# Optimization experiments

Hardware: AMD Instinct MI355X
Metric: run time of the kernel (lower is better)

The kernel has to match this reference:

```python
import jax, jax.numpy as jnp
import numpy as np

NEAR = 0.01
FAR = 10.0
MAX_ITERS = 32
N_RAYS = 65536
HIDDEN = 128


def setup_inputs() -> dict:
    key = jax.random.key(0)
    ks = jax.random.split(key, 12)
    f = jnp.float32
    origins = jax.random.normal(ks[0], (N_RAYS, 3), f) * 2.0
    directions = jax.random.normal(ks[1], (N_RAYS, 3), f)
    directions = directions / jnp.linalg.norm(directions, axis=-1, keepdims=True)
    s1 = 1.0 / np.sqrt(3.0)
    s2 = 1.0 / np.sqrt(HIDDEN)
    return {
        "origins": origins,
        "directions": directions,
        "W1": jax.random.normal(ks[2], (3, HIDDEN), f) * s1,
        "b1": jax.random.normal(ks[3], (HIDDEN,), f) * 0.01,
        "W2": jax.random.normal(ks[4], (HIDDEN, HIDDEN), f) * s2,
        "b2": jax.random.normal(ks[5], (HIDDEN,), f) * 0.01,
        "W3": jax.random.normal(ks[6], (HIDDEN, 1), f) * s2,
        "b3": jax.random.normal(ks[7], (1,), f) * 0.01,
        "Wc1": jax.random.normal(ks[8], (3, HIDDEN), f) * s1,
        "bc1": jax.random.normal(ks[9], (HIDDEN,), f) * 0.01,
        "Wc2": jax.random.normal(ks[10], (HIDDEN, 3), f) * s2,
        "bc2": jax.random.normal(ks[11], (3,), f) * 0.01,
    }


def reference(origins, directions, W1, b1, W2, b2, W3, b3, Wc1, bc1, Wc2, bc2):
    N = origins.shape[0]

    def sdf(p):  # [N,3] -> [N,1]
        h = jax.nn.relu(p @ W1 + b1)
        h = jax.nn.relu(h @ W2 + b2)
        return h @ W3 + b3

    def get_color(p):  # [N,3] -> [N,3]
        h = jax.nn.relu(p @ Wc1 + bc1)
        return jax.nn.sigmoid(h @ Wc2 + bc2)

    def step(state, _):
        points, distances, final_mask = state
        sdfs = sdf(points)                                  # [N,1]
        valid = (sdfs <= NEAR) & (distances < FAR)          # [N,1] bool
        final_mask = final_mask | valid
        upd = ~valid                                        # rays still marching
        distances = distances + jnp.where(upd, sdfs, 0.0)
        points = points + jnp.where(upd, directions * sdfs, 0.0)
        return (points, distances, final_mask), None

    init = (origins,
            jnp.zeros((N, 1), origins.dtype),
            jnp.zeros((N, 1), dtype=bool))
    (points, distances, final_mask), _ = jax.lax.scan(step, init, None, length=MAX_ITERS)
    final_mask = final_mask | (distances < FAR)             # [N,1]

    # color[mask] = get_color(points[mask]) <=> masked where (get_color is pointwise)
    color = jnp.where(final_mask, get_color(points), 0.0)   # [N,3]
    return color
```

## Files before the change

kernel.cpp:

```cpp
#include <hip/hip_runtime.h>

#define HIDDEN 128
#define N_RAYS 65536
#define NEAR_D 0.01f
#define FAR_D 10.0f
#define MAX_ITERS 32

typedef _Float16 f16x8 __attribute__((ext_vector_type(8)));
typedef float f32x16 __attribute__((ext_vector_type(16)));

template <int CTRL, int ROW_MASK>
__device__ __forceinline__ float dpp_add(float v) {
    int s = __builtin_amdgcn_update_dpp(0, __float_as_int(v), CTRL, ROW_MASK, 0xF, true);
    return v + __int_as_float(s);
}
__device__ __forceinline__ float half_sum_dpp(float v) {
    v = dpp_add<0x111, 0xF>(v);
    v = dpp_add<0x112, 0xF>(v);
    v = dpp_add<0x114, 0xF>(v);
    v = dpp_add<0x118, 0xF>(v);
    v = dpp_add<0x142, 0xA>(v);
    return v;
}

__global__ void w2_frag_kernel(const float* __restrict__ W2,
                               _Float16* __restrict__ img) {
    int tid = blockIdx.x * blockDim.x + threadIdx.x;
    int j = tid & 7;
    int L = (tid >> 3) & 63;
    int tc = tid >> 9;
    int t = tc >> 3, c = tc & 7;
    int n = t * 32 + (L & 31);
    int k = c * 16 + ((L >> 5) & 1) * 8 + j;
    float w = W2[k * HIDDEN + n];
    _Float16 hi = (_Float16)w;
    _Float16 lo = (_Float16)(w - (float)hi);
    img[tid] = hi;
    img[16384 + tid] = lo;
}

__launch_bounds__(256, 2)
__global__ void sphere_trace_kernel(
    const float* __restrict__ origins,
    const float* __restrict__ directions,
    const float* __restrict__ W1,
    const float* __restrict__ b1,
    const _Float16* __restrict__ w2img,
    const float* __restrict__ b2,
    const float* __restrict__ W3,
    const float* __restrict__ b3,
    const float* __restrict__ Wc1,
    const float* __restrict__ bc1,
    const float* __restrict__ Wc2,
    const float* __restrict__ bc2,
    float* __restrict__ out)
{
    __shared__ __align__(16) _Float16 wlds[32768];
    __shared__ float sbuf[4][32];

    const int tid = threadIdx.x;
    const int lane = tid & 63;
    const int w = __builtin_amdgcn_readfirstlane(tid >> 6);
    const int q = lane >> 5;
    const int n32 = lane & 31;

    {
        const float4* src = (const float4*)w2img;
        float4* dst = (float4*)wlds;
        #pragma unroll
        for (int i = 0; i < 16; ++i)
            dst[tid + 256 * i] = src[tid + 256 * i];
    }
    __syncthreads();

    float bAx, bAy, bAz, bB;
    {
        bAx = fmaxf(fabsf(W1[lane]),              fabsf(W1[lane + 64]));
        bAy = fmaxf(fabsf(W1[HIDDEN + lane]),     fabsf(W1[HIDDEN + lane + 64]));
        bAz = fmaxf(fabsf(W1[2 * HIDDEN + lane]), fabsf(W1[2 * HIDDEN + lane + 64]));
        bB  = fmaxf(fabsf(b1[lane]),              fabsf(b1[lane + 64]));
        #pragma unroll
        for (int m = 1; m < 64; m <<= 1) {
            bAx = fmaxf(bAx, __shfl_xor(bAx, m));
            bAy = fmaxf(bAy, __shfl_xor(bAy, m));
            bAz = fmaxf(bAz, __shfl_xor(bAz, m));
            bB  = fmaxf(bB,  __shfl_xor(bB,  m));
        }
    }

    const int ray = blockIdx.x * 128 + w * 32 + n32;
    float px = 0.f, py = 0.f, pz = 0.f, dx = 0.f, dy = 0.f, dz = 0.f;
    float dist = 0.0f;
    bool frozen = true;
    if (lane < 32) {
        px = origins[ray * 3 + 0];
        py = origins[ray * 3 + 1];
        pz = origins[ray * 3 + 2];
        dx = directions[ray * 3 + 0];
        dy = directions[ray * 3 + 1];
        dz = directions[ray * 3 + 2];
        frozen = false;
    }

    float b2v[4], w3v[4];
    #pragma unroll
    for (int t = 0; t < 4; ++t) {
        b2v[t] = b2[t * 32 + n32];
        w3v[t] = W3[t * 32 + n32];
    }
    const float b3v = b3[0];
    const int q8 = q * 8;

    #pragma unroll 1
    for (int it = 0; it < MAX_ITERS; ++it) {
        const float ppx = __shfl(px, n32);
        const float ppy = __shfl(py, n32);
        const float ppz = __shfl(pz, n32);

        const float bound = fmaf(fabsf(ppx), bAx, fmaf(fabsf(ppy), bAy,
                            fmaf(fabsf(ppz), bAz, bB)));
        float sc = 1.0f, inv = 1.0f;
        {
            const int e = (int)((__float_as_uint(bound) >> 23) & 255u);
            if (e > 137) {
                const int sh = e - 137;
                sc  = __uint_as_float((unsigned)(127 - sh) << 23);
                inv = __uint_as_float((unsigned)(127 + sh) << 23);
            }
        }

        f32x16 acc[4];
        #pragma unroll
        for (int t = 0; t < 4; ++t)
            #pragma unroll
            for (int r = 0; r < 16; ++r) acc[t][r] = 0.0f;

        #pragma unroll 1
        for (int c = 0; c < 8; ++c) {
            f16x8 Ah, Al;
            {
                const int kb = c * 16 + q8;
                const float* wpx = W1 + kb;
                const float* wpy = W1 + HIDDEN + kb;
                const float* wpz = W1 + 2 * HIDDEN + kb;
                const float* bp  = b1 + kb;
                #pragma unroll
                for (int jj = 0; jj < 8; ++jj) {
                    const float hv = fmaxf(
                        fmaf(ppx, wpx[jj], fmaf(ppy, wpy[jj],
                        fmaf(ppz, wpz[jj], bp[jj]))), 0.0f);
                    const float x = hv * sc;
                    const _Float16 hi = (_Float16)x;
                    Ah[jj] = hi;
                    Al[jj] = (_Float16)(x - (float)hi);
                }
            }
            #pragma unroll
            for (int t = 0; t < 4; ++t) {
                const int off = ((t * 8 + c) << 9) + (lane << 3);
                const f16x8 bh = *(const f16x8*)(wlds + off);
                const f16x8 bl = *(const f16x8*)(wlds + 16384 + off);
                acc[t] = __builtin_amdgcn_mfma_f32_32x32x16_f16(Ah, bh, acc[t], 0, 0, 0);
                acc[t] = __builtin_amdgcn_mfma_f32_32x32x16_f16(Ah, bl, acc[t], 0, 0, 0);
                acc[t] = __builtin_amdgcn_mfma_f32_32x32x16_f16(Al, bh, acc[t], 0, 0, 0);
            }
        }

        float invr[16];
        #pragma unroll
        for (int r = 0; r < 16; ++r) {
            const int msrc = (r & 3) + 8 * (r >> 2) + 4 * q;
            invr[r] = __shfl(inv, msrc);
        }
        float ps[16];
        #pragma unroll
        for (int r = 0; r < 16; ++r) ps[r] = 0.0f;
        #pragma unroll
        for (int t = 0; t < 4; ++t) {
            #pragma unroll
            for (int r = 0; r < 16; ++r) {
                const float v = fmaxf(fmaf(acc[t][r], invr[r], b2v[t]), 0.0f);
                ps[r] = fmaf(v, w3v[t], ps[r]);
            }
        }

        #pragma unroll
        for (int r = 0; r < 16; ++r)
            ps[r] = half_sum_dpp(ps[r]);
        if ((lane & 31) == 31) {
            const int mb = q * 4;
            #pragma unroll
            for (int g = 0; g < 4; ++g) {
                float4 v4;
                v4.x = ps[4 * g + 0];
                v4.y = ps[4 * g + 1];
                v4.z = ps[4 * g + 2];
                v4.w = ps[4 * g + 3];
                *(float4*)&sbuf[w][8 * g + mb] = v4;
            }
        }
        float s = 0.0f;
        if (lane < 32) s = sbuf[w][lane] + b3v;

        if (lane < 32) {
            const bool valid = (s <= NEAR_D) && (dist < FAR_D);
            if (!frozen) {
                if (valid) {
                    frozen = true;
                } else {
                    dist += s;
                    px = fmaf(dx, s, px);
                    py = fmaf(dy, s, py);
                    pz = fmaf(dz, s, pz);
                }
            }
        }
        if (__ballot((lane < 32) && !frozen) == 0) break;
    }

    const int k0 = lane, k1 = lane + 64;
    const float cx0 = Wc1[k0], cx1 = Wc1[k1];
    const float cy0 = Wc1[HIDDEN + k0], cy1 = Wc1[HIDDEN + k1];
    const float cz0 = Wc1[2 * HIDDEN + k0], cz1 = Wc1[2 * HIDDEN + k1];
    const float cb0 = bc1[k0], cb1 = bc1[k1];
    const float u00 = Wc2[k0 * 3 + 0], u01 = Wc2[k0 * 3 + 1], u02 = Wc2[k0 * 3 + 2];
    const float u10 = Wc2[k1 * 3 + 0], u11 = Wc2[k1 * 3 + 1], u12 = Wc2[k1 * 3 + 2];

    float g0 = 0.f, g1 = 0.f, g2 = 0.f;
    #pragma unroll 1
    for (int m = 0; m < 32; ++m) {
        const float qx = __shfl(px, m);
        const float qy = __shfl(py, m);
        const float qz = __shfl(pz, m);
        const float h0 = fmaxf(fmaf(qx, cx0, fmaf(qy, cy0, fmaf(qz, cz0, cb0))), 0.f);
        const float h1 = fmaxf(fmaf(qx, cx1, fmaf(qy, cy1, fmaf(qz, cz1, cb1))), 0.f);
        float a0 = fmaf(h0, u00, h1 * u10);
        float a1 = fmaf(h0, u01, h1 * u11);
        float a2 = fmaf(h0, u02, h1 * u12);
        #pragma unroll
        for (int mask = 1; mask < 64; mask <<= 1) {
            a0 += __shfl_xor(a0, mask);
            a1 += __shfl_xor(a1, mask);
            a2 += __shfl_xor(a2, mask);
        }
        if (lane == m) { g0 = a0; g1 = a1; g2 = a2; }
    }

    if (lane < 32) {
        float c0 = 0.f, c1 = 0.f, c2 = 0.f;
        if (frozen || dist < FAR_D) {
            c0 = 1.0f / (1.0f + __expf(-(g0 + bc2[0])));
            c1 = 1.0f / (1.0f + __expf(-(g1 + bc2[1])));
            c2 = 1.0f / (1.0f + __expf(-(g2 + bc2[2])));
        }
        out[ray * 3 + 0] = c0;
        out[ray * 3 + 1] = c1;
        out[ray * 3 + 2] = c2;
    }
}

extern "C" void kernel_launch(void* const* d_in, const int* in_sizes, int n_in,
                              void* d_out, int out_size, void* d_ws, size_t ws_size,
                              hipStream_t stream) {
    const float* origins    = (const float*)d_in[0];
    const float* directions = (const float*)d_in[1];
    const float* W1  = (const float*)d_in[2];
    const float* b1  = (const float*)d_in[3];
    const float* W2  = (const float*)d_in[4];
    const float* b2  = (const float*)d_in[5];
    const float* W3  = (const float*)d_in[6];
    const float* b3  = (const float*)d_in[7];
    const float* Wc1 = (const float*)d_in[8];
    const float* bc1 = (const float*)d_in[9];
    const float* Wc2 = (const float*)d_in[10];
    const float* bc2 = (const float*)d_in[11];
    float* out = (float*)d_out;

    _Float16* w2img = (_Float16*)d_ws;

    w2_frag_kernel<<<64, 256, 0, stream>>>(W2, w2img);

    sphere_trace_kernel<<<N_RAYS / 128, 256, 0, stream>>>(
        origins, directions, W1, b1, w2img, b2, W3, b3,
        Wc1, bc1, Wc2, bc2, out);
}
```

Measured before the change: 306.2 us.

## Split marching into two phases with compaction of still-active rays

Marching is split into two kernels. The first runs 8 iterations for every ray, colours the rays that have already converged, and appends the still-marching rays with their state to a compacted list through an atomic counter. The second kernel runs the remaining iterations only on the compacted rays, so waves are densely populated and blocks past the count exit early. This reduces divergence waste from waves held alive by a few slow rays, at the cost of an extra launch, state writes and reads, restaging the weights, and running the colour MLP in both phases.

```diff
diff --git a/kernel.cpp b/kernel.cpp
--- a/kernel.cpp
+++ b/kernel.cpp
@@ -5,6 +5,8 @@
 #define NEAR_D 0.01f
 #define FAR_D 10.0f
 #define MAX_ITERS 32
+#define P1_ITERS 8
+#define P2_ITERS (MAX_ITERS - P1_ITERS)
 
 typedef _Float16 f16x8 __attribute__((ext_vector_type(8)));
 typedef float f32x16 __attribute__((ext_vector_type(16)));
@@ -24,8 +26,10 @@
 }
 
 __global__ void w2_frag_kernel(const float* __restrict__ W2,
-                               _Float16* __restrict__ img) {
+                               _Float16* __restrict__ img,
+                               int* __restrict__ scount) {
     int tid = blockIdx.x * blockDim.x + threadIdx.x;
+    if (blockIdx.x == 0 && threadIdx.x == 0) *scount = 0;
     int j = tid & 7;
     int L = (tid >> 3) & 63;
     int tc = tid >> 9;
@@ -39,80 +43,18 @@
     img[16384 + tid] = lo;
 }
 
-__launch_bounds__(256, 2)
-__global__ void sphere_trace_kernel(
-    const float* __restrict__ origins,
-    const float* __restrict__ directions,
-    const float* __restrict__ W1,
-    const float* __restrict__ b1,
-    const _Float16* __restrict__ w2img,
-    const float* __restrict__ b2,
-    const float* __restrict__ W3,
-    const float* __restrict__ b3,
-    const float* __restrict__ Wc1,
-    const float* __restrict__ bc1,
-    const float* __restrict__ Wc2,
-    const float* __restrict__ bc2,
-    float* __restrict__ out)
+__device__ __forceinline__ void march_loop(
+    const int iters, const int lane, const int q, const int n32,
+    const _Float16* wlds, float* swave,
+    const float* __restrict__ W1, const float* __restrict__ b1,
+    const float* b2v, const float* w3v, const float b3v,
+    const float bAx, const float bAy, const float bAz, const float bB,
+    const float dx, const float dy, const float dz,
+    float& px, float& py, float& pz, float& dist, bool& frozen)
 {
-    __shared__ __align__(16) _Float16 wlds[32768];
-    __shared__ float sbuf[4][32];
-
-    const int tid = threadIdx.x;
-    const int lane = tid & 63;
-    const int w = __builtin_amdgcn_readfirstlane(tid >> 6);
-    const int q = lane >> 5;
-    const int n32 = lane & 31;
-
-    {
-        const float4* src = (const float4*)w2img;
-        float4* dst = (float4*)wlds;
-        #pragma unroll
-        for (int i = 0; i < 16; ++i)
-            dst[tid + 256 * i] = src[tid + 256 * i];
-    }
-    __syncthreads();
-
-    float bAx, bAy, bAz, bB;
-    {
-        bAx = fmaxf(fabsf(W1[lane]),              fabsf(W1[lane + 64]));
-        bAy = fmaxf(fabsf(W1[HIDDEN + lane]),     fabsf(W1[HIDDEN + lane + 64]));
-        bAz = fmaxf(fabsf(W1[2 * HIDDEN + lane]), fabsf(W1[2 * HIDDEN + lane + 64]));
-        bB  = fmaxf(fabsf(b1[lane]),              fabsf(b1[lane + 64]));
-        #pragma unroll
-        for (int m = 1; m < 64; m <<= 1) {
-            bAx = fmaxf(bAx, __shfl_xor(bAx, m));
-            bAy = fmaxf(bAy, __shfl_xor(bAy, m));
-            bAz = fmaxf(bAz, __shfl_xor(bAz, m));
-            bB  = fmaxf(bB,  __shfl_xor(bB,  m));
-        }
-    }
-
-    const int ray = blockIdx.x * 128 + w * 32 + n32;
-    float px = 0.f, py = 0.f, pz = 0.f, dx = 0.f, dy = 0.f, dz = 0.f;
-    float dist = 0.0f;
-    bool frozen = true;
-    if (lane < 32) {
-        px = origins[ray * 3 + 0];
-        py = origins[ray * 3 + 1];
-        pz = origins[ray * 3 + 2];
-        dx = directions[ray * 3 + 0];
-        dy = directions[ray * 3 + 1];
-        dz = directions[ray * 3 + 2];
-        frozen = false;
-    }
-
-    float b2v[4], w3v[4];
-    #pragma unroll
-    for (int t = 0; t < 4; ++t) {
-        b2v[t] = b2[t * 32 + n32];
-        w3v[t] = W3[t * 32 + n32];
-    }
-    const float b3v = b3[0];
     const int q8 = q * 8;
-
     #pragma unroll 1
-    for (int it = 0; it < MAX_ITERS; ++it) {
+    for (int it = 0; it < iters; ++it) {
         const float ppx = __shfl(px, n32);
         const float ppy = __shfl(py, n32);
         const float ppz = __shfl(pz, n32);
@@ -196,11 +138,11 @@
                 v4.y = ps[4 * g + 1];
                 v4.z = ps[4 * g + 2];
                 v4.w = ps[4 * g + 3];
-                *(float4*)&sbuf[w][8 * g + mb] = v4;
+                *(float4*)&swave[8 * g + mb] = v4;
             }
         }
         float s = 0.0f;
-        if (lane < 32) s = sbuf[w][lane] + b3v;
+        if (lane < 32) s = swave[lane] + b3v;
 
         if (lane < 32) {
             const bool valid = (s <= NEAR_D) && (dist < FAR_D);
@@ -217,7 +159,14 @@
         }
         if (__ballot((lane < 32) && !frozen) == 0) break;
     }
-
+}
+
+__device__ __forceinline__ void color_mlp(
+    const int lane, const float px, const float py, const float pz,
+    const float* __restrict__ Wc1, const float* __restrict__ bc1,
+    const float* __restrict__ Wc2,
+    float& g0, float& g1, float& g2)
+{
     const int k0 = lane, k1 = lane + 64;
     const float cx0 = Wc1[k0], cx1 = Wc1[k1];
     const float cy0 = Wc1[HIDDEN + k0], cy1 = Wc1[HIDDEN + k1];
@@ -226,7 +175,7 @@
     const float u00 = Wc2[k0 * 3 + 0], u01 = Wc2[k0 * 3 + 1], u02 = Wc2[k0 * 3 + 2];
     const float u10 = Wc2[k1 * 3 + 0], u11 = Wc2[k1 * 3 + 1], u12 = Wc2[k1 * 3 + 2];
 
-    float g0 = 0.f, g1 = 0.f, g2 = 0.f;
+    g0 = 0.f; g1 = 0.f; g2 = 0.f;
     #pragma unroll 1
     for (int m = 0; m < 32; ++m) {
         const float qx = __shfl(px, m);
@@ -245,8 +194,164 @@
         }
         if (lane == m) { g0 = a0; g1 = a1; g2 = a2; }
     }
-
+}
+
+#define WAVE_SETUP()                                                          \
+    float bAx, bAy, bAz, bB;                                                  \
+    {                                                                         \
+        bAx = fmaxf(fabsf(W1[lane]),              fabsf(W1[lane + 64]));      \
+        bAy = fmaxf(fabsf(W1[HIDDEN + lane]),     fabsf(W1[HIDDEN + lane + 64])); \
+        bAz = fmaxf(fabsf(W1[2 * HIDDEN + lane]), fabsf(W1[2 * HIDDEN + lane + 64])); \
+        bB  = fmaxf(fabsf(b1[lane]),              fabsf(b1[lane + 64]));      \
+        _Pragma("unroll")                                                     \
+        for (int m = 1; m < 64; m <<= 1) {                                    \
+            bAx = fmaxf(bAx, __shfl_xor(bAx, m));                             \
+            bAy = fmaxf(bAy, __shfl_xor(bAy, m));                             \
+            bAz = fmaxf(bAz, __shfl_xor(bAz, m));                             \
+            bB  = fmaxf(bB,  __shfl_xor(bB,  m));                             \
+        }                                                                     \
+    }                                                                         \
+    float b2v[4], w3v[4];                                                     \
+    _Pragma("unroll")                                                         \
+    for (int t = 0; t < 4; ++t) {                                             \
+        b2v[t] = b2[t * 32 + n32];                                            \
+        w3v[t] = W3[t * 32 + n32];                                            \
+    }                                                                         \
+    const float b3v = b3[0];
+
+#define STAGE_WLDS()                                                          \
+    {                                                                         \
+        const float4* src = (const float4*)w2img;                             \
+        float4* dst = (float4*)wlds;                                          \
+        _Pragma("unroll")                                                     \
+        for (int i = 0; i < 16; ++i)                                          \
+            dst[tid + 256 * i] = src[tid + 256 * i];                          \
+    }                                                                         \
+    __syncthreads();
+
+__launch_bounds__(256, 2)
+__global__ void phase1_kernel(
+    const float* __restrict__ origins, const float* __restrict__ directions,
+    const float* __restrict__ W1, const float* __restrict__ b1,
+    const _Float16* __restrict__ w2img,
+    const float* __restrict__ b2, const float* __restrict__ W3,
+    const float* __restrict__ b3,
+    const float* __restrict__ Wc1, const float* __restrict__ bc1,
+    const float* __restrict__ Wc2, const float* __restrict__ bc2,
+    float* __restrict__ out,
+    float4* __restrict__ state, int* __restrict__ slist,
+    int* __restrict__ scount)
+{
+    __shared__ __align__(16) _Float16 wlds[32768];
+    __shared__ float sbuf[4][32];
+
+    const int tid = threadIdx.x;
+    const int lane = tid & 63;
+    const int w = __builtin_amdgcn_readfirstlane(tid >> 6);
+    const int q = lane >> 5;
+    const int n32 = lane & 31;
+
+    STAGE_WLDS();
+    WAVE_SETUP();
+
+    const int ray = blockIdx.x * 128 + w * 32 + n32;
+    float px = 0.f, py = 0.f, pz = 0.f, dx = 0.f, dy = 0.f, dz = 0.f;
+    float dist = 0.0f;
+    bool frozen = true;
     if (lane < 32) {
+        px = origins[ray * 3 + 0];
+        py = origins[ray * 3 + 1];
+        pz = origins[ray * 3 + 2];
+        dx = directions[ray * 3 + 0];
+        dy = directions[ray * 3 + 1];
+        dz = directions[ray * 3 + 2];
+        frozen = false;
+    }
+
+    march_loop(P1_ITERS, lane, q, n32, wlds, &sbuf[w][0],
+               W1, b1, b2v, w3v, b3v, bAx, bAy, bAz, bB,
+               dx, dy, dz, px, py, pz, dist, frozen);
+
+    const bool active = (lane < 32) && !frozen;
+    if (active) {
+        float4 st; st.x = px; st.y = py; st.z = pz; st.w = dist;
+        state[ray] = st;
+    }
+    {
+        const unsigned long long mb = __ballot(active);
+        const int cnt = __popcll(mb);
+        if (cnt) {
+            const int leader = __ffsll(mb) - 1;
+            int base = 0;
+            if (lane == leader) base = atomicAdd(scount, cnt);
+            base = __shfl(base, leader);
+            if (active) {
+                const int pos = __popcll(mb & ((1ull << lane) - 1ull));
+                slist[base + pos] = ray;
+            }
+        }
+    }
+
+    float g0, g1, g2;
+    color_mlp(lane, px, py, pz, Wc1, bc1, Wc2, g0, g1, g2);
+    if ((lane < 32) && frozen) {
+        out[ray * 3 + 0] = 1.0f / (1.0f + __expf(-(g0 + bc2[0])));
+        out[ray * 3 + 1] = 1.0f / (1.0f + __expf(-(g1 + bc2[1])));
+        out[ray * 3 + 2] = 1.0f / (1.0f + __expf(-(g2 + bc2[2])));
+    }
+}
+
+__launch_bounds__(256, 2)
+__global__ void phase2_kernel(
+    const float* __restrict__ directions,
+    const float* __restrict__ W1, const float* __restrict__ b1,
+    const _Float16* __restrict__ w2img,
+    const float* __restrict__ b2, const float* __restrict__ W3,
+    const float* __restrict__ b3,
+    const float* __restrict__ Wc1, const float* __restrict__ bc1,
+    const float* __restrict__ Wc2, const float* __restrict__ bc2,
+    float* __restrict__ out,
+    const float4* __restrict__ state, const int* __restrict__ slist,
+    const int* __restrict__ scount)
+{
+    __shared__ __align__(16) _Float16 wlds[32768];
+    __shared__ float sbuf[4][32];
+
+    const int count = *scount;
+    if (blockIdx.x * 128 >= count) return;
+
+    const int tid = threadIdx.x;
+    const int lane = tid & 63;
+    const int w = __builtin_amdgcn_readfirstlane(tid >> 6);
+    const int q = lane >> 5;
+    const int n32 = lane & 31;
+
+    STAGE_WLDS();
+    WAVE_SETUP();
+
+    const int slot = blockIdx.x * 128 + w * 32 + n32;
+    const bool live = (lane < 32) && (slot < count);
+    int ray = 0;
+    float px = 0.f, py = 0.f, pz = 0.f, dx = 0.f, dy = 0.f, dz = 0.f;
+    float dist = 1.0e9f;
+    bool frozen = true;
+    if (live) {
+        ray = slist[slot];
+        const float4 st = state[ray];
+        px = st.x; py = st.y; pz = st.z; dist = st.w;
+        dx = directions[ray * 3 + 0];
+        dy = directions[ray * 3 + 1];
+        dz = directions[ray * 3 + 2];
+        frozen = false;
+    }
+
+    march_loop(P2_ITERS, lane, q, n32, wlds, &sbuf[w][0],
+               W1, b1, b2v, w3v, b3v, bAx, bAy, bAz, bB,
+               dx, dy, dz, px, py, pz, dist, frozen);
+
+    float g0, g1, g2;
+    color_mlp(lane, px, py, pz, Wc1, bc1, Wc2, g0, g1, g2);
+    if (live) {
         float c0 = 0.f, c1 = 0.f, c2 = 0.f;
         if (frozen || dist < FAR_D) {
             c0 = 1.0f / (1.0f + __expf(-(g0 + bc2[0])));
@@ -276,11 +381,19 @@
     const float* bc2 = (const float*)d_in[11];
     float* out = (float*)d_out;
 
-    _Float16* w2img = (_Float16*)d_ws;
-
-    w2_frag_kernel<<<64, 256, 0, stream>>>(W2, w2img);
-
-    sphere_trace_kernel<<<N_RAYS / 128, 256, 0, stream>>>(
+    char* ws = (char*)d_ws;
+    _Float16* w2img = (_Float16*)ws;
+    int*      scount = (int*)(ws + 65536);
+    int*      slist  = (int*)(ws + 65536 + 256);
+    float4*   state  = (float4*)(ws + 65536 + 256 + 262144);
+
+    w2_frag_kernel<<<64, 256, 0, stream>>>(W2, w2img, scount);
+
+    phase1_kernel<<<N_RAYS / 128, 256, 0, stream>>>(
         origins, directions, W1, b1, w2img, b2, W3, b3,
-        Wc1, bc1, Wc2, bc2, out);
-}
+        Wc1, bc1, Wc2, bc2, out, state, slist, scount);
+
+    phase2_kernel<<<N_RAYS / 128, 256, 0, stream>>>(
+        directions, W1, b1, w2img, b2, W3, b3,
+        Wc1, bc1, Wc2, bc2, out, state, slist, scount);
+}
```

After: 346.2 us. 13.1% more time.
